# Kernel tuning notes

Hardware: AMD Instinct MI355X
Metric: run time of the kernel (lower is better)

## Reference

```python
import jax, jax.numpy as jnp
import numpy as np

B, S, D = 4, 2048, 1024


def setup_inputs() -> dict:
    key = jax.random.key(0)
    k1, k2, k3, k4 = jax.random.split(key, 4)
    scale = 1.0 / np.sqrt(D)
    return {
        "X_emb": jax.random.normal(k1, (B, S, D), dtype=jnp.float32),
        "W_q": jax.random.normal(k2, (D, D), dtype=jnp.float32) * scale,
        "W_k": jax.random.normal(k3, (D, D), dtype=jnp.float32) * scale,
        "W_v": jax.random.normal(k4, (D, D), dtype=jnp.float32) * scale,
    }


def reference(X_emb, W_q, W_k, W_v):
    # nn.Linear(bias=False): x @ W.T
    Xq = jnp.einsum('bsd,ed->bse', X_emb, W_q)
    Xk = jnp.einsum('bsd,ed->bse', X_emb, W_k)
    Xv = jnp.einsum('bsd,ed->bse', X_emb, W_v)
    S_len = X_emb.shape[-2]
    # scores [B, S, S]; causal mask (strict upper triangle -> -inf)
    att = jnp.einsum('bqe,bke->bqk', Xq, Xk)
    causal = jnp.tril(jnp.ones((S_len, S_len), dtype=bool))
    att = jnp.where(causal, att, -jnp.inf)
    # note: original masks before scaling; -inf / sqrt(d) is still -inf
    att = att / jnp.sqrt(jnp.asarray(Xk.shape[-1], att.dtype))
    w = jax.nn.softmax(att, axis=-1)
    return jnp.einsum('bqk,bke->bqe', w, Xv)
```

## Files before the change

### kernel.cpp

```cpp
#include <hip/hip_runtime.h>
#include <stdint.h>
#include <math.h>

typedef __attribute__((ext_vector_type(8))) __bf16 bf16x8;
typedef __attribute__((ext_vector_type(4))) float f32x4;

__device__ __forceinline__ unsigned short f2bf(float f) {
    unsigned u = __float_as_uint(f);
    u += 0x7FFF + ((u >> 16) & 1);
    return (unsigned short)(u >> 16);
}
__device__ __forceinline__ float bf2f(unsigned short u) {
    return __uint_as_float((unsigned)u << 16);
}

__global__ __launch_bounds__(256)
void convt_k(const float* __restrict__ X, const float* __restrict__ Wq,
             const float* __restrict__ Wk, const float* __restrict__ Wv,
             unsigned short* __restrict__ Xb, unsigned short* __restrict__ WqT,
             unsigned short* __restrict__ WkT, unsigned short* __restrict__ Wvb,
             float* __restrict__ outz) {
    const int S = 2048, D = 1024;
    const int z = blockIdx.z;
    const int t = threadIdx.x;
    if (z == 7) {
        const int n4 = 4 * S * D / 4 * 4 / 4;
        int gid = (blockIdx.y * 16 + blockIdx.x) * 256 + t;
        int stride = 512 * 256;
        float4 zz = (float4){0.f, 0.f, 0.f, 0.f};
        for (int i = gid; i < 4 * S * D / 4; i += stride)
            reinterpret_cast<float4*>(outz)[i] = zz;
        return;
    }
    const float* src;
    unsigned short* dstP = nullptr;
    unsigned short* dstT = nullptr;
    int rows;
    if (z < 4)      { src = X + (size_t)z * S * D; dstP = Xb + (size_t)z * S * D; rows = S; }
    else if (z == 4){ src = Wq; dstT = WqT; rows = D; }
    else if (z == 5){ src = Wk; dstT = WkT; rows = D; }
    else            { src = Wv; dstP = Wvb; rows = D; }
    const int r0 = blockIdx.y * 64, c0 = blockIdx.x * 64;
    if (r0 >= rows) return;

    __shared__ float tile[64][65];
    const int tr = t >> 4;
    const int tc4 = t & 15;
#pragma unroll
    for (int p = 0; p < 4; ++p) {
        int r = p * 16 + tr;
        float4 v = *reinterpret_cast<const float4*>(&src[(size_t)(r0 + r) * 1024 + c0 + tc4 * 4]);
        if (dstP) {
            ushort4 o; o.x = f2bf(v.x); o.y = f2bf(v.y); o.z = f2bf(v.z); o.w = f2bf(v.w);
            *reinterpret_cast<ushort4*>(&dstP[(size_t)(r0 + r) * 1024 + c0 + tc4 * 4]) = o;
        }
        if (dstT) {
            tile[r][tc4 * 4 + 0] = v.x; tile[r][tc4 * 4 + 1] = v.y;
            tile[r][tc4 * 4 + 2] = v.z; tile[r][tc4 * 4 + 3] = v.w;
        }
    }
    if (!dstT) return;
    __syncthreads();
#pragma unroll
    for (int p = 0; p < 4; ++p) {
        int c = p * 16 + tr;
        ushort4 o;
        o.x = f2bf(tile[tc4 * 4 + 0][c]);
        o.y = f2bf(tile[tc4 * 4 + 1][c]);
        o.z = f2bf(tile[tc4 * 4 + 2][c]);
        o.w = f2bf(tile[tc4 * 4 + 3][c]);
        *reinterpret_cast<ushort4*>(&dstT[(size_t)(c0 + c) * 1024 + r0 + tc4 * 4]) = o;
    }
}

__global__ __launch_bounds__(256)
void reduce4_k(const float* __restrict__ p, unsigned short* __restrict__ o, int n4) {
    const int slab = 1024 * 1024 / 4;
    int i = blockIdx.x * blockDim.x + threadIdx.x;
    int stride = gridDim.x * blockDim.x;
    for (; i < n4; i += stride) {
        float4 a = reinterpret_cast<const float4*>(p)[i];
        float4 b = reinterpret_cast<const float4*>(p)[i + slab];
        float4 c = reinterpret_cast<const float4*>(p)[i + 2 * slab];
        float4 d = reinterpret_cast<const float4*>(p)[i + 3 * slab];
        ushort4 u;
        u.x = f2bf(a.x + b.x + c.x + d.x);
        u.y = f2bf(a.y + b.y + c.y + d.y);
        u.z = f2bf(a.z + b.z + c.z + d.z);
        u.w = f2bf(a.w + b.w + c.w + d.w);
        reinterpret_cast<ushort4*>(o)[i] = u;
    }
}

__device__ __forceinline__ void gload16(const unsigned short* g, unsigned short* l) {
    __builtin_amdgcn_global_load_lds(
        (const __attribute__((address_space(1))) unsigned int*)g,
        (__attribute__((address_space(3))) unsigned int*)l, 16, 0, 0);
}

template <typename CT, bool ATOMIC>
__device__ __forceinline__ void core_tile(
    const unsigned short* __restrict__ A, const unsigned short* __restrict__ B,
    CT* __restrict__ C, int lda, int ldb, int ldc,
    int m0, int n0, int kst, int nk, float scale, bool first,
    unsigned short* AsB, unsigned short* BsB)
{
    const int t    = threadIdx.x;
    const int lane = t & 63;
    const int wid  = t >> 6;
    const int wm   = wid >> 1, wn = wid & 1;
    const int rsel = lane & 15;
    const int gsel = lane >> 4;
    const int srow = t >> 3;
    const int swz  = ((t & 7) ^ (srow & 7)) * 8;

    f32x4 acc[4][4];
#pragma unroll
    for (int m = 0; m < 4; ++m)
#pragma unroll
        for (int n = 0; n < 4; ++n) acc[m][n] = (f32x4){0.f, 0.f, 0.f, 0.f};

    const unsigned short* gpA[4];
    const unsigned short* gpB[4];
#pragma unroll
    for (int i = 0; i < 4; ++i) {
        gpA[i] = A + (long long)(m0 + srow + 32 * i) * lda + kst * 64 + swz;
        gpB[i] = B + (long long)(n0 + srow + 32 * i) * ldb + kst * 64 + swz;
    }

    auto stage = [&](int buf) {
#pragma unroll
        for (int i = 0; i < 4; ++i)
            gload16(gpA[i], &AsB[buf * 8192 + i * 2048 + t * 8]);
#pragma unroll
        for (int i = 0; i < 4; ++i)
            gload16(gpB[i], &BsB[buf * 8192 + i * 2048 + t * 8]);
#pragma unroll
        for (int i = 0; i < 4; ++i) { gpA[i] += 64; gpB[i] += 64; }
    };

    if (!first) {
        __builtin_amdgcn_s_barrier();
        __builtin_amdgcn_sched_barrier(0);
    }
    stage(0);

    for (int kt = 0; kt < nk; ++kt) {
        const int c = kt & 1;
        __builtin_amdgcn_s_barrier();
        __builtin_amdgcn_sched_barrier(0);
        if (kt + 1 < nk) {
            stage(c ^ 1);
            asm volatile("s_waitcnt vmcnt(8)" ::: "memory");
        } else {
            asm volatile("s_waitcnt vmcnt(0)" ::: "memory");
        }
        __builtin_amdgcn_s_barrier();
        __builtin_amdgcn_sched_barrier(0);

        bf16x8 aF[4][2], bF[4][2];
#pragma unroll
        for (int m = 0; m < 4; ++m)
#pragma unroll
            for (int ks = 0; ks < 2; ++ks) {
                int r  = wm * 64 + m * 16 + rsel;
                int cc = ks * 4 + gsel;
                aF[m][ks] = *reinterpret_cast<const bf16x8*>(
                    &AsB[c * 8192 + r * 64 + ((cc ^ (r & 7)) * 8)]);
            }
#pragma unroll
        for (int n = 0; n < 4; ++n)
#pragma unroll
            for (int ks = 0; ks < 2; ++ks) {
                int rb = wn * 64 + n * 16 + rsel;
                int cc = ks * 4 + gsel;
                bF[n][ks] = *reinterpret_cast<const bf16x8*>(
                    &BsB[c * 8192 + rb * 64 + ((cc ^ (rb & 7)) * 8)]);
            }

        __builtin_amdgcn_s_setprio(1);
#pragma unroll
        for (int m = 0; m < 4; ++m)
#pragma unroll
            for (int n = 0; n < 4; ++n)
#pragma unroll
                for (int ks = 0; ks < 2; ++ks)
                    acc[m][n] = __builtin_amdgcn_mfma_f32_16x16x32_bf16(
                        aF[m][ks], bF[n][ks], acc[m][n], 0, 0, 0);
        __builtin_amdgcn_s_setprio(0);
    }

    const int rowl = gsel * 4;
#pragma unroll
    for (int m = 0; m < 4; ++m)
#pragma unroll
        for (int n = 0; n < 4; ++n)
#pragma unroll
            for (int i = 0; i < 4; ++i) {
                int r  = m0 + wm * 64 + m * 16 + rowl + i;
                int cI = n0 + wn * 64 + n * 16 + rsel;
                float v = acc[m][n][i] * scale;
                if constexpr (sizeof(CT) == 2)
                    ((unsigned short*)C)[(long long)r * ldc + cI] = f2bf(v);
                else if constexpr (ATOMIC)
                    unsafeAtomicAdd((float*)&C[(long long)r * ldc + cI], v);
                else
                    ((float*)C)[(long long)r * ldc + cI] = v;
            }
}

__device__ __forceinline__ void tri_decode(int w, int& br, int& bc) {
    int rr = (int)((sqrtf(8.0f * (float)w + 1.0f) - 1.0f) * 0.5f);
    while ((rr + 1) * (rr + 2) / 2 <= w) ++rr;
    while (rr * (rr + 1) / 2 > w) --rr;
    br = rr; bc = w - rr * (rr + 1) / 2;
}

template <typename CT>
__global__ __launch_bounds__(256, 2)
void gemm0(const unsigned short* __restrict__ A, const unsigned short* __restrict__ B,
           CT* __restrict__ C, int lda, int ldb, int ldc, int K,
           long long sA, long long sB, long long sC, float scale)
{
    __shared__ unsigned short As[2 * 8192];
    __shared__ unsigned short Bs[2 * 8192];
    const int nbx = gridDim.x;
    const int nwg = nbx * gridDim.y;
    const int orig = blockIdx.y * nbx + blockIdx.x;
    const int q8 = nwg >> 3, r8 = nwg & 7;
    const int xcd = orig & 7, idx = orig >> 3;
    const int work = (xcd < r8 ? xcd * (q8 + 1) : r8 * (q8 + 1) + (xcd - r8) * q8) + idx;
    core_tile<CT, false>(A + (long long)blockIdx.z * sA, B + (long long)blockIdx.z * sB,
                         C + (long long)blockIdx.z * sC, lda, ldb, ldc,
                         (work / nbx) * 128, (work % nbx) * 128, 0, K >> 6, scale, true,
                         As, Bs);
}

__global__ __launch_bounds__(256, 2)
void gemm_mrg(const unsigned short* __restrict__ XM, const unsigned short* __restrict__ Xb,
              unsigned short* __restrict__ Sc, const unsigned short* __restrict__ Wv,
              unsigned short* __restrict__ Vt)
{
    const int S = 2048, D = 1024;
    const long long SD = (long long)S * D, SS = (long long)S * S, DS = (long long)D * S;
    __shared__ unsigned short As[2 * 8192];
    __shared__ unsigned short Bs[2 * 8192];
    const int orig = blockIdx.x;
    const int work = (orig & 7) * 128 + (orig >> 3);
    const int xcdc = work >> 7, idx = work & 127;

    if (idx < 4) {
        int d = xcdc * 4 + idx;
        int b = d >> 3, dp = d & 7;
        const unsigned short* A = XM + b * SD;
        const unsigned short* B = Xb + b * SD;
        unsigned short* C = Sc + b * SS;
        core_tile<unsigned short, false>(A, B, C, D, D, S,
            (2 * dp) * 128, (2 * dp) * 128, 0, 16, 0.03125f, true, As, Bs);
        core_tile<unsigned short, false>(A, B, C, D, D, S,
            (2 * dp + 1) * 128, (2 * dp + 1) * 128, 0, 16, 0.03125f, false, As, Bs);
    } else {
        int j = xcdc * 124 + (idx - 4);
        if (j < 480) {
            int b = j / 120, tt = j % 120;
            int rr, cc;
            tri_decode(tt, rr, cc);
            int br = rr + 1, bc = tt - rr * (rr + 1) / 2;
            core_tile<unsigned short, false>(XM + b * SD, Xb + b * SD, Sc + b * SS,
                D, D, S, br * 128, bc * 128, 0, 16, 0.03125f, true, As, Bs);
        } else {
            int v = j - 480;
            int b = v >> 7, u = v & 127;
            int r = u >> 4, c = u & 15;
            core_tile<unsigned short, false>(Wv, Xb + b * SD, Vt + b * DS,
                D, D, S, r * 128, c * 128, 0, 16, 1.0f, true, As, Bs);
        }
    }
}

__global__ __launch_bounds__(256, 2)
void gemm_pv(const unsigned short* __restrict__ P, const unsigned short* __restrict__ Vt,
             float* __restrict__ out)
{
    const int S = 2048, D = 1024;
    const long long SS = (long long)S * S, DS = (long long)D * S, SD = (long long)S * D;
    __shared__ unsigned short As[2 * 8192];
    __shared__ unsigned short Bs[2 * 8192];
    const int orig = blockIdx.x;
    const int work = (orig & 7) * 96 + (orig >> 3);
    if (work < 512) {
        int b = work >> 7, u = work & 127;
        int r = 8 + (u >> 4);
        int rest = u & 15;
        int c = rest >> 1, h = rest & 1;
        int nk = r + 1;
        core_tile<float, true>(P + b * SS, Vt + b * DS, out + b * SD,
            S, S, D, r * 128, c * 128, h * nk, nk, 1.0f, true, As, Bs);
    } else {
        int a = work - 512;
        int b = a >> 6, u = a & 63;
        int r = u >> 3, c = u & 7;
        core_tile<float, false>(P + b * SS, Vt + b * DS, out + b * SD,
            S, S, D, r * 128, c * 128, 0, 2 * (r + 1), 1.0f, true, As, Bs);
    }
}

__device__ __forceinline__ float waveMax(float v) {
#pragma unroll
    for (int o = 32; o > 0; o >>= 1) v = fmaxf(v, __shfl_xor(v, o, 64));
    return v;
}
__device__ __forceinline__ float waveSum(float v) {
#pragma unroll
    for (int o = 32; o > 0; o >>= 1) v += __shfl_xor(v, o, 64);
    return v;
}

__global__ __launch_bounds__(256)
void softmax_causal(const unsigned short* __restrict__ S, unsigned short* __restrict__ P,
                    int Slen) {
    __shared__ float e[2048];
    __shared__ float red[4];
    long long row = blockIdx.x;
    int q = (int)(row % Slen);
    const unsigned short* srow = S + row * (long long)Slen;
    unsigned short* prow = P + row * (long long)Slen;
    int len = q + 1;
    int t = threadIdx.x;

    int n8 = len >> 3;
    float mx = -3.0e38f;
    for (int i = t; i < n8; i += 256) {
        uint4 v = reinterpret_cast<const uint4*>(srow)[i];
        float f0 = __uint_as_float(v.x << 16), f1 = __uint_as_float(v.x & 0xffff0000u);
        float f2 = __uint_as_float(v.y << 16), f3 = __uint_as_float(v.y & 0xffff0000u);
        float f4 = __uint_as_float(v.z << 16), f5 = __uint_as_float(v.z & 0xffff0000u);
        float f6 = __uint_as_float(v.w << 16), f7 = __uint_as_float(v.w & 0xffff0000u);
        e[8 * i + 0] = f0; e[8 * i + 1] = f1; e[8 * i + 2] = f2; e[8 * i + 3] = f3;
        e[8 * i + 4] = f4; e[8 * i + 5] = f5; e[8 * i + 6] = f6; e[8 * i + 7] = f7;
        mx = fmaxf(mx, fmaxf(fmaxf(fmaxf(f0, f1), fmaxf(f2, f3)),
                             fmaxf(fmaxf(f4, f5), fmaxf(f6, f7))));
    }
    if (t < (len & 7)) {
        float v = bf2f(srow[n8 * 8 + t]);
        e[n8 * 8 + t] = v;
        mx = fmaxf(mx, v);
    }
    mx = waveMax(mx);
    if ((t & 63) == 0) red[t >> 6] = mx;
    __syncthreads();
    mx = fmaxf(fmaxf(red[0], red[1]), fmaxf(red[2], red[3]));

    float sum = 0.f;
    for (int k = t; k < len; k += 256) {
        float v = __expf(e[k] - mx);
        e[k] = v;
        sum += v;
    }
    sum = waveSum(sum);
    __syncthreads();
    if ((t & 63) == 0) red[t >> 6] = sum;
    __syncthreads();
    sum = red[0] + red[1] + red[2] + red[3];
    float inv = 1.0f / sum;

    int wlim = ((q >> 7) + 1) << 7;
    __syncthreads();
    for (int i = t; i < (wlim >> 2); i += 256) {
        int k = 4 * i;
        ushort4 o;
        o.x = (k + 0 < len) ? f2bf(e[k + 0] * inv) : (unsigned short)0;
        o.y = (k + 1 < len) ? f2bf(e[k + 1] * inv) : (unsigned short)0;
        o.z = (k + 2 < len) ? f2bf(e[k + 2] * inv) : (unsigned short)0;
        o.w = (k + 3 < len) ? f2bf(e[k + 3] * inv) : (unsigned short)0;
        reinterpret_cast<ushort4*>(prow)[i] = o;
    }
}

extern "C" void kernel_launch(void* const* d_in, const int* in_sizes, int n_in,
                              void* d_out, int out_size, void* d_ws, size_t ws_size,
                              hipStream_t stream) {
    const int B = 4, S = 2048, D = 1024;
    const float* X  = (const float*)d_in[0];
    const float* Wq = (const float*)d_in[1];
    const float* Wk = (const float*)d_in[2];
    const float* Wv = (const float*)d_in[3];
    float* out = (float*)d_out;

    char* ws = (char*)d_ws;
    unsigned short* Xb    = (unsigned short*)ws; ws += (size_t)B * S * D * 2;
    unsigned short* WqT   = (unsigned short*)ws; ws += (size_t)D * D * 2;
    unsigned short* WkT   = (unsigned short*)ws; ws += (size_t)D * D * 2;
    unsigned short* Wvb   = (unsigned short*)ws; ws += (size_t)D * D * 2;
    unsigned short* MTb   = (unsigned short*)ws; ws += (size_t)D * D * 2;
    unsigned short* XMb   = (unsigned short*)ws; ws += (size_t)B * S * D * 2;
    unsigned short* Vt    = (unsigned short*)ws; ws += (size_t)B * D * S * 2;
    unsigned short* Sc    = (unsigned short*)ws; ws += (size_t)B * S * S * 2;
    unsigned short* P     = (unsigned short*)ws; ws += (size_t)B * S * S * 2;
    float*          Mpart = (float*)ws;          ws += (size_t)4 * D * D * 4;

    convt_k<<<dim3(16, 32, 8), 256, 0, stream>>>(X, Wq, Wk, Wv, Xb, WqT, WkT, Wvb, out);

    dim3 blk(256);
    gemm0<float><<<dim3(8, 8, 4), blk, 0, stream>>>(
        WkT, WqT, Mpart, D, D, D, 256, 256, 256, (long long)D * D, 1.0f);
    reduce4_k<<<1024, 256, 0, stream>>>(Mpart, MTb, D * D / 4);

    gemm0<unsigned short><<<dim3(8, 64, 1), blk, 0, stream>>>(
        Xb, MTb, XMb, D, D, D, D, 0, 0, 0, 1.0f);

    gemm_mrg<<<dim3(1024, 1, 1), blk, 0, stream>>>(XMb, Xb, Sc, Wvb, Vt);

    softmax_causal<<<B * S, 256, 0, stream>>>(Sc, P, S);

    gemm_pv<<<dim3(768, 1, 1), blk, 0, stream>>>(P, Vt, out);
}
```

Measured before the change: 163.3 us.

## Regroup GEMM launches: fuse XM with V projection, split causal score GEMM, reorder PV tiles

Moves the XM = X·M GEMM into the same launch as the V-projection GEMM, giving one 1024-block launch. The causal score GEMM becomes its own 544-block launch over the lower-triangular tiles, including the diagonal. The PV kernel now dispatches tiles longest-first, so heavy split-K rows start before light ones. The aim is better load balance and fewer under-filled launches, at the cost of an extra dependency boundary between the XM/V launch and the score launch.

```diff
diff --git a/kernel.cpp b/kernel.cpp
--- a/kernel.cpp
+++ b/kernel.cpp
@@ -24,7 +24,6 @@
     const int z = blockIdx.z;
     const int t = threadIdx.x;
     if (z == 7) {
-        const int n4 = 4 * S * D / 4 * 4 / 4;
         int gid = (blockIdx.y * 16 + blockIdx.x) * 256 + t;
         int stride = 512 * 256;
         float4 zz = (float4){0.f, 0.f, 0.f, 0.f};
@@ -237,45 +236,44 @@
 }
 
 __global__ __launch_bounds__(256, 2)
-void gemm_mrg(const unsigned short* __restrict__ XM, const unsigned short* __restrict__ Xb,
-              unsigned short* __restrict__ Sc, const unsigned short* __restrict__ Wv,
-              unsigned short* __restrict__ Vt)
+void gemm_xmvt(const unsigned short* __restrict__ Xb, const unsigned short* __restrict__ MTb,
+               unsigned short* __restrict__ XMb, const unsigned short* __restrict__ Wv,
+               unsigned short* __restrict__ Vt)
 {
     const int S = 2048, D = 1024;
-    const long long SD = (long long)S * D, SS = (long long)S * S, DS = (long long)D * S;
+    const long long SD = (long long)S * D, DS = (long long)D * S;
     __shared__ unsigned short As[2 * 8192];
     __shared__ unsigned short Bs[2 * 8192];
     const int orig = blockIdx.x;
     const int work = (orig & 7) * 128 + (orig >> 3);
-    const int xcdc = work >> 7, idx = work & 127;
-
-    if (idx < 4) {
-        int d = xcdc * 4 + idx;
-        int b = d >> 3, dp = d & 7;
-        const unsigned short* A = XM + b * SD;
-        const unsigned short* B = Xb + b * SD;
-        unsigned short* C = Sc + b * SS;
-        core_tile<unsigned short, false>(A, B, C, D, D, S,
-            (2 * dp) * 128, (2 * dp) * 128, 0, 16, 0.03125f, true, As, Bs);
-        core_tile<unsigned short, false>(A, B, C, D, D, S,
-            (2 * dp + 1) * 128, (2 * dp + 1) * 128, 0, 16, 0.03125f, false, As, Bs);
+    if (work < 512) {
+        int rw = work >> 3, c = work & 7;
+        core_tile<unsigned short, false>(Xb, MTb, XMb, D, D, D,
+            rw * 128, c * 128, 0, 16, 1.0f, true, As, Bs);
     } else {
-        int j = xcdc * 124 + (idx - 4);
-        if (j < 480) {
-            int b = j / 120, tt = j % 120;
-            int rr, cc;
-            tri_decode(tt, rr, cc);
-            int br = rr + 1, bc = tt - rr * (rr + 1) / 2;
-            core_tile<unsigned short, false>(XM + b * SD, Xb + b * SD, Sc + b * SS,
-                D, D, S, br * 128, bc * 128, 0, 16, 0.03125f, true, As, Bs);
-        } else {
-            int v = j - 480;
-            int b = v >> 7, u = v & 127;
-            int r = u >> 4, c = u & 15;
-            core_tile<unsigned short, false>(Wv, Xb + b * SD, Vt + b * DS,
-                D, D, S, r * 128, c * 128, 0, 16, 1.0f, true, As, Bs);
-        }
-    }
+        int v = work - 512;
+        int b = v >> 7, u = v & 127;
+        int r = u >> 4, c = u & 15;
+        core_tile<unsigned short, false>(Wv, Xb + b * SD, Vt + b * DS, D, D, S,
+            r * 128, c * 128, 0, 16, 1.0f, true, As, Bs);
+    }
+}
+
+__global__ __launch_bounds__(256, 2)
+void gemm_sc(const unsigned short* __restrict__ XM, const unsigned short* __restrict__ Xb,
+             unsigned short* __restrict__ Sc)
+{
+    const int S = 2048, D = 1024;
+    const long long SD = (long long)S * D, SS = (long long)S * S;
+    __shared__ unsigned short As[2 * 8192];
+    __shared__ unsigned short Bs[2 * 8192];
+    const int orig = blockIdx.x;
+    const int work = (orig & 7) * 68 + (orig >> 3);
+    int b = work / 136, tt = work % 136;
+    int br, bc;
+    tri_decode(tt, br, bc);
+    core_tile<unsigned short, false>(XM + b * SD, Xb + b * SD, Sc + b * SS,
+        D, D, S, br * 128, bc * 128, 0, 16, 0.03125f, true, As, Bs);
 }
 
 __global__ __launch_bounds__(256, 2)
@@ -286,22 +284,20 @@
     const long long SS = (long long)S * S, DS = (long long)D * S, SD = (long long)S * D;
     __shared__ unsigned short As[2 * 8192];
     __shared__ unsigned short Bs[2 * 8192];
-    const int orig = blockIdx.x;
-    const int work = (orig & 7) * 96 + (orig >> 3);
-    if (work < 512) {
-        int b = work >> 7, u = work & 127;
-        int r = 8 + (u >> 4);
-        int rest = u & 15;
-        int c = rest >> 1, h = rest & 1;
-        int nk = r + 1;
-        core_tile<float, true>(P + b * SS, Vt + b * DS, out + b * SD,
-            S, S, D, r * 128, c * 128, h * nk, nk, 1.0f, true, As, Bs);
+    const int cnt[16]  = {64,32,64,64,32,64,64,32,64,64,32,64,32,32,32,32};
+    const int rowt[16] = {15, 7,14,13, 6,12,11, 5,10, 9, 4, 8, 3, 2, 1, 0};
+    const int isB[16]  = { 1, 0, 1, 1, 0, 1, 1, 0, 1, 1, 0, 1, 0, 0, 0, 0};
+    int w = blockIdx.x, k = 0;
+    while (w >= cnt[k]) { w -= cnt[k]; ++k; }
+    const int r = rowt[k];
+    if (isB[k]) {
+        int b = w >> 4, u = w & 15, c = u >> 1, h = u & 1;
+        core_tile<float, true>(P + b * SS, Vt + b * DS, out + b * SD, S, S, D,
+            r * 128, c * 128, h * (r + 1), r + 1, 1.0f, true, As, Bs);
     } else {
-        int a = work - 512;
-        int b = a >> 6, u = a & 63;
-        int r = u >> 3, c = u & 7;
-        core_tile<float, false>(P + b * SS, Vt + b * DS, out + b * SD,
-            S, S, D, r * 128, c * 128, 0, 2 * (r + 1), 1.0f, true, As, Bs);
+        int b = w >> 3, c = w & 7;
+        core_tile<float, false>(P + b * SS, Vt + b * DS, out + b * SD, S, S, D,
+            r * 128, c * 128, 0, 2 * (r + 1), 1.0f, true, As, Bs);
     }
 }
 
@@ -406,10 +402,9 @@
         WkT, WqT, Mpart, D, D, D, 256, 256, 256, (long long)D * D, 1.0f);
     reduce4_k<<<1024, 256, 0, stream>>>(Mpart, MTb, D * D / 4);
 
-    gemm0<unsigned short><<<dim3(8, 64, 1), blk, 0, stream>>>(
-        Xb, MTb, XMb, D, D, D, D, 0, 0, 0, 1.0f);
-
-    gemm_mrg<<<dim3(1024, 1, 1), blk, 0, stream>>>(XMb, Xb, Sc, Wvb, Vt);
+    gemm_xmvt<<<dim3(1024, 1, 1), blk, 0, stream>>>(Xb, MTb, XMb, Wvb, Vt);
+
+    gemm_sc<<<dim3(544, 1, 1), blk, 0, stream>>>(XMb, Xb, Sc);
 
     softmax_causal<<<B * S, 256, 0, stream>>>(Sc, P, S);
 
```

Measured after the change: 169.0 us. +3.5%, slower.
